# Optimization experiments

Measured on AMD Instinct MI355X. Metric: run time of the kernel, lower is better.

The kernel has to match this reference:

```python
import jax, jax.numpy as jnp
import numpy as np

MIN_VAL = 1e-12  # Ln(min_val=1e-12) in MorphLayer
KSIZE = 3
STRIDE = 1


def _patches(x, k, s):
    # x: (B, C, H, W) -> (B, C*k*k, Ho, Wo), im2col like torch unfold
    return jax.lax.conv_general_dilated_patches(x, (k, k), (s, s), 'VALID')


def _max_plus(p, w):
    # log-domain morphological conv: (B, K, Ho, Wo) + (K, F) -> max over K -> (B, F, Ho, Wo)
    return jnp.max(p[:, :, None, :, :] + w[None, :, :, None, None], axis=1)


def setup_inputs() -> dict:
    key = jax.random.key(0)
    k1, k2, k3 = jax.random.split(key, 3)
    B, C, H, W = 16, 3, 66, 66
    F = 32
    K = C * KSIZE * KSIZE  # 27
    return {
        'x': jax.random.normal(k1, (B, C, H, W), dtype=jnp.float32),
        'kernel_k1': jax.random.normal(k2, (K, F), dtype=jnp.float32) * 0.1,
        'kernel_k2': jax.random.normal(k3, (K, F), dtype=jnp.float32) * 0.1,
        'bias': jnp.zeros((F,), dtype=jnp.float32),
    }


def reference(x, kernel_k1, kernel_k2, bias):
    # Ln: log of positive / negative parts, clamped at MIN_VAL
    x1 = jnp.log(jnp.maximum(x, MIN_VAL))
    x2 = jnp.log(jnp.maximum(-x, MIN_VAL))
    p1 = _patches(x1, KSIZE, STRIDE)  # (B, K, Ho, Wo)
    p2 = _patches(x2, KSIZE, STRIDE)
    y11 = jnp.exp(_max_plus(p1, kernel_k1))
    y12 = jnp.exp(_max_plus(p1, kernel_k2))
    y21 = jnp.exp(_max_plus(p2, kernel_k1))
    y22 = jnp.exp(_max_plus(p2, kernel_k2))
    return y11 - y12 - y21 + y22 + bias[None, :, None, None]
```

## Files before the change

kernel.cpp:

```cpp
#include <hip/hip_runtime.h>
#include <math.h>


#define BB 16
#define CC 3
#define HH 66
#define WW 66
#define HO 64
#define WO 64
#define FF 32
#define KK 27
#define FPB 4
#define FG (FF / FPB)
#define ROWS 4
#define IR (ROWS + 2)
#define LP 68
#define WSTRIDE 56

typedef float f32x2 __attribute__((ext_vector_type(2)));
typedef float f32x4 __attribute__((ext_vector_type(4)));

__global__ __launch_bounds__(256, 8)
void morph_tile(const float* __restrict__ x,
                const float* __restrict__ k1,
                const float* __restrict__ k2,
                const float* __restrict__ bias,
                float* __restrict__ out) {
    __shared__ __align__(16) float xs[CC * IR * LP];
    __shared__ __align__(16) float wl[FPB * WSTRIDE];

    const int tid = threadIdx.x;
    int bid = blockIdx.x;
    const int fg = bid & (FG - 1); bid >>= 3;
    const int rb = bid & 15;       bid >>= 4;
    const int b  = bid;
    const int f0 = fg * FPB;
    const int ho0 = rb * ROWS;

    if (tid < FPB * KK * 2) {
        const int w_  = tid / (KK * 2);
        const int rem = tid - w_ * (KK * 2);
        const int k   = rem >> 1;
        const int h   = rem & 1;
        const float wv = h ? k2[k * FF + f0 + w_] : k1[k * FF + f0 + w_];
        wl[w_ * WSTRIDE + k * 2 + h] = expf(wv);
    }
    const float* xbase = x + (size_t)b * CC * HH * WW;
    for (int i = tid; i < CC * IR * WW; i += 256) {
        const int c   = i / (IR * WW);
        const int rem = i - c * (IR * WW);
        const int row = rem / WW;
        const int col = rem - row * WW;
        xs[(c * IR + row) * LP + col] = xbase[(c * HH + ho0 + row) * WW + col];
    }
    __syncthreads();

    const int w   = tid >> 6;
    const int l   = tid & 63;
    const int rr  = l >> 4;
    const int wo4 = (l & 15) * 4;

    const float* wlw = wl + w * WSTRIDE;
    const int f = f0 + w;

    float m11_0 = 0.f, m11_1 = 0.f, m11_2 = 0.f, m11_3 = 0.f;
    float m12_0 = 0.f, m12_1 = 0.f, m12_2 = 0.f, m12_3 = 0.f;
    float m21_0 = 0.f, m21_1 = 0.f, m21_2 = 0.f, m21_3 = 0.f;
    float m22_0 = 0.f, m22_1 = 0.f, m22_2 = 0.f, m22_3 = 0.f;

#define TAP(k, va, vb, vc, vd) { \
        const f32x2 e = *(const f32x2*)(wlw + (k) * 2);   \
        const f32x2 ab = {va, vb}, cd = {vc, vd}; \
        const f32x2 e1 = {e.x, e.x}, e2 = {e.y, e.y}; \
        const f32x2 p1 = ab * e1, q1 = cd * e1; \
        const f32x2 p2 = ab * e2, q2 = cd * e2; \
        m11_0 = fmaxf(m11_0,  p1.x); m11_1 = fmaxf(m11_1,  p1.y); \
        m11_2 = fmaxf(m11_2,  q1.x); m11_3 = fmaxf(m11_3,  q1.y); \
        m12_0 = fmaxf(m12_0,  p2.x); m12_1 = fmaxf(m12_1,  p2.y); \
        m12_2 = fmaxf(m12_2,  q2.x); m12_3 = fmaxf(m12_3,  q2.y); \
        m21_0 = fmaxf(m21_0, -p1.x); m21_1 = fmaxf(m21_1, -p1.y); \
        m21_2 = fmaxf(m21_2, -q1.x); m21_3 = fmaxf(m21_3, -q1.y); \
        m22_0 = fmaxf(m22_0, -p2.x); m22_1 = fmaxf(m22_1, -p2.y); \
        m22_2 = fmaxf(m22_2, -q2.x); m22_3 = fmaxf(m22_3, -q2.y); \
    }

#define CHUNK(c, di) { \
        const int base_ = ((c * IR + rr + (di)) * LP + wo4); \
        const f32x4 xq = *(const f32x4*)(xs + base_); \
        const f32x2 xr = *(const f32x2*)(xs + base_ + 4); \
        const float s0 = xq.x, s1 = xq.y, s2 = xq.z, s3 = xq.w; \
        const float s4 = xr.x, s5 = xr.y; \
        TAP((c) * 9 + (di) * 3 + 0, s0, s1, s2, s3) \
        TAP((c) * 9 + (di) * 3 + 1, s1, s2, s3, s4) \
        TAP((c) * 9 + (di) * 3 + 2, s2, s3, s4, s5) \
    }

    CHUNK(0, 0) CHUNK(0, 1) CHUNK(0, 2)
    CHUNK(1, 0) CHUNK(1, 1) CHUNK(1, 2)
    CHUNK(2, 0) CHUNK(2, 1) CHUNK(2, 2)
#undef CHUNK
#undef TAP

    const float bs = bias[f];
    f32x4 res;
    res.x = m11_0 - m12_0 - m21_0 + m22_0 + bs;
    res.y = m11_1 - m12_1 - m21_1 + m22_1 + bs;
    res.z = m11_2 - m12_2 - m21_2 + m22_2 + bs;
    res.w = m11_3 - m12_3 - m21_3 + m22_3 + bs;

    *(f32x4*)(out + (((size_t)b * FF + f) * HO + ho0 + rr) * WO + wo4) = res;
}

extern "C" void kernel_launch(void* const* d_in, const int* in_sizes, int n_in,
                              void* d_out, int out_size, void* d_ws, size_t ws_size,
                              hipStream_t stream) {
    const float* x    = (const float*)d_in[0];
    const float* k1   = (const float*)d_in[1];
    const float* k2   = (const float*)d_in[2];
    const float* bias = (const float*)d_in[3];
    float* out = (float*)d_out;

    const int nblocks = BB * (HO / ROWS) * FG;
    morph_tile<<<dim3(nblocks), dim3(256), 0, stream>>>(x, k1, k2, bias, out);
}
```

Before: 14.73 us.

## Compute two output rows per thread with per-channel register window and paired taps

Each thread now computes two output rows instead of one, so a block covers eight rows and half as many blocks are launched. Per channel, the thread loads a 4x8 window from shared memory into registers once and reuses it across both rows and all nine taps. Taps are processed in pairs with nested fmax to shorten dependency chains. This cuts shared-memory loads and per-block staging overhead, but raises register use (launch bounds occupancy hint lowered to 4) and halves grid parallelism.

```diff
diff --git a/kernel.cpp b/kernel.cpp
--- a/kernel.cpp
+++ b/kernel.cpp
@@ -12,15 +12,15 @@
 #define KK 27
 #define FPB 4
 #define FG (FF / FPB)
-#define ROWS 4
-#define IR (ROWS + 2)
+#define OROWS 8
+#define IR (OROWS + 2)
 #define LP 68
 #define WSTRIDE 56
 
 typedef float f32x2 __attribute__((ext_vector_type(2)));
 typedef float f32x4 __attribute__((ext_vector_type(4)));
 
-__global__ __launch_bounds__(256, 8)
+__global__ __launch_bounds__(256, 4)
 void morph_tile(const float* __restrict__ x,
                 const float* __restrict__ k1,
                 const float* __restrict__ k2,
@@ -32,10 +32,10 @@
     const int tid = threadIdx.x;
     int bid = blockIdx.x;
     const int fg = bid & (FG - 1); bid >>= 3;
-    const int rb = bid & 15;       bid >>= 4;
+    const int rb = bid & 7;        bid >>= 3;
     const int b  = bid;
     const int f0 = fg * FPB;
-    const int ho0 = rb * ROWS;
+    const int ho0 = rb * OROWS;
 
     if (tid < FPB * KK * 2) {
         const int w_  = tid / (KK * 2);
@@ -57,58 +57,123 @@
 
     const int w   = tid >> 6;
     const int l   = tid & 63;
-    const int rr  = l >> 4;
+    const int rq  = l >> 4;
     const int wo4 = (l & 15) * 4;
+    const int r0  = rq * 2;
 
     const float* wlw = wl + w * WSTRIDE;
     const int f = f0 + w;
 
-    float m11_0 = 0.f, m11_1 = 0.f, m11_2 = 0.f, m11_3 = 0.f;
-    float m12_0 = 0.f, m12_1 = 0.f, m12_2 = 0.f, m12_3 = 0.f;
-    float m21_0 = 0.f, m21_1 = 0.f, m21_2 = 0.f, m21_3 = 0.f;
-    float m22_0 = 0.f, m22_1 = 0.f, m22_2 = 0.f, m22_3 = 0.f;
+    float m11[2][4], m12[2][4], m21[2][4], m22[2][4];
+    #pragma unroll
+    for (int h = 0; h < 2; ++h)
+        #pragma unroll
+        for (int j = 0; j < 4; ++j) {
+            m11[h][j] = 0.f; m12[h][j] = 0.f; m21[h][j] = 0.f; m22[h][j] = 0.f;
+        }
 
-#define TAP(k, va, vb, vc, vd) { \
-        const f32x2 e = *(const f32x2*)(wlw + (k) * 2);   \
-        const f32x2 ab = {va, vb}, cd = {vc, vd}; \
-        const f32x2 e1 = {e.x, e.x}, e2 = {e.y, e.y}; \
-        const f32x2 p1 = ab * e1, q1 = cd * e1; \
-        const f32x2 p2 = ab * e2, q2 = cd * e2; \
-        m11_0 = fmaxf(m11_0,  p1.x); m11_1 = fmaxf(m11_1,  p1.y); \
-        m11_2 = fmaxf(m11_2,  q1.x); m11_3 = fmaxf(m11_3,  q1.y); \
-        m12_0 = fmaxf(m12_0,  p2.x); m12_1 = fmaxf(m12_1,  p2.y); \
-        m12_2 = fmaxf(m12_2,  q2.x); m12_3 = fmaxf(m12_3,  q2.y); \
-        m21_0 = fmaxf(m21_0, -p1.x); m21_1 = fmaxf(m21_1, -p1.y); \
-        m21_2 = fmaxf(m21_2, -q1.x); m21_3 = fmaxf(m21_3, -q1.y); \
-        m22_0 = fmaxf(m22_0, -p2.x); m22_1 = fmaxf(m22_1, -p2.y); \
-        m22_2 = fmaxf(m22_2, -q2.x); m22_3 = fmaxf(m22_3, -q2.y); \
+    float xw[4][8];
+
+#define LOADCH(c) { \
+        const float* xc_ = xs + ((c) * IR + r0) * LP + wo4; \
+        *(f32x4*)&xw[0][0] = *(const f32x4*)(xc_); \
+        *(f32x4*)&xw[0][4] = *(const f32x4*)(xc_ + 4); \
+        *(f32x4*)&xw[1][0] = *(const f32x4*)(xc_ + LP); \
+        *(f32x4*)&xw[1][4] = *(const f32x4*)(xc_ + LP + 4); \
+        *(f32x4*)&xw[2][0] = *(const f32x4*)(xc_ + 2 * LP); \
+        *(f32x4*)&xw[2][4] = *(const f32x4*)(xc_ + 2 * LP + 4); \
+        *(f32x4*)&xw[3][0] = *(const f32x4*)(xc_ + 3 * LP); \
+        *(f32x4*)&xw[3][4] = *(const f32x4*)(xc_ + 3 * LP + 4); \
     }
 
-#define CHUNK(c, di) { \
-        const int base_ = ((c * IR + rr + (di)) * LP + wo4); \
-        const f32x4 xq = *(const f32x4*)(xs + base_); \
-        const f32x2 xr = *(const f32x2*)(xs + base_ + 4); \
-        const float s0 = xq.x, s1 = xq.y, s2 = xq.z, s3 = xq.w; \
-        const float s4 = xr.x, s5 = xr.y; \
-        TAP((c) * 9 + (di) * 3 + 0, s0, s1, s2, s3) \
-        TAP((c) * 9 + (di) * 3 + 1, s1, s2, s3, s4) \
-        TAP((c) * 9 + (di) * 3 + 2, s2, s3, s4, s5) \
+#define TP_H(h, Ai, Aj, Bi, Bj, e1A, e2A, e1B, e2B) { \
+        const f32x2 pA1 = (f32x2){xw[(Ai)+(h)][(Aj)],   xw[(Ai)+(h)][(Aj)+1]} * e1A; \
+        const f32x2 qA1 = (f32x2){xw[(Ai)+(h)][(Aj)+2], xw[(Ai)+(h)][(Aj)+3]} * e1A; \
+        const f32x2 pA2 = (f32x2){xw[(Ai)+(h)][(Aj)],   xw[(Ai)+(h)][(Aj)+1]} * e2A; \
+        const f32x2 qA2 = (f32x2){xw[(Ai)+(h)][(Aj)+2], xw[(Ai)+(h)][(Aj)+3]} * e2A; \
+        const f32x2 pB1 = (f32x2){xw[(Bi)+(h)][(Bj)],   xw[(Bi)+(h)][(Bj)+1]} * e1B; \
+        const f32x2 qB1 = (f32x2){xw[(Bi)+(h)][(Bj)+2], xw[(Bi)+(h)][(Bj)+3]} * e1B; \
+        const f32x2 pB2 = (f32x2){xw[(Bi)+(h)][(Bj)],   xw[(Bi)+(h)][(Bj)+1]} * e2B; \
+        const f32x2 qB2 = (f32x2){xw[(Bi)+(h)][(Bj)+2], xw[(Bi)+(h)][(Bj)+3]} * e2B; \
+        m11[h][0] = fmaxf(fmaxf(m11[h][0],  pA1.x),  pB1.x); \
+        m11[h][1] = fmaxf(fmaxf(m11[h][1],  pA1.y),  pB1.y); \
+        m11[h][2] = fmaxf(fmaxf(m11[h][2],  qA1.x),  qB1.x); \
+        m11[h][3] = fmaxf(fmaxf(m11[h][3],  qA1.y),  qB1.y); \
+        m12[h][0] = fmaxf(fmaxf(m12[h][0],  pA2.x),  pB2.x); \
+        m12[h][1] = fmaxf(fmaxf(m12[h][1],  pA2.y),  pB2.y); \
+        m12[h][2] = fmaxf(fmaxf(m12[h][2],  qA2.x),  qB2.x); \
+        m12[h][3] = fmaxf(fmaxf(m12[h][3],  qA2.y),  qB2.y); \
+        m21[h][0] = fmaxf(fmaxf(m21[h][0], -pA1.x), -pB1.x); \
+        m21[h][1] = fmaxf(fmaxf(m21[h][1], -pA1.y), -pB1.y); \
+        m21[h][2] = fmaxf(fmaxf(m21[h][2], -qA1.x), -qB1.x); \
+        m21[h][3] = fmaxf(fmaxf(m21[h][3], -qA1.y), -qB1.y); \
+        m22[h][0] = fmaxf(fmaxf(m22[h][0], -pA2.x), -pB2.x); \
+        m22[h][1] = fmaxf(fmaxf(m22[h][1], -pA2.y), -pB2.y); \
+        m22[h][2] = fmaxf(fmaxf(m22[h][2], -qA2.x), -qB2.x); \
+        m22[h][3] = fmaxf(fmaxf(m22[h][3], -qA2.y), -qB2.y); \
     }
 
-    CHUNK(0, 0) CHUNK(0, 1) CHUNK(0, 2)
-    CHUNK(1, 0) CHUNK(1, 1) CHUNK(1, 2)
-    CHUNK(2, 0) CHUNK(2, 1) CHUNK(2, 2)
-#undef CHUNK
-#undef TAP
+#define TAPPAIR(Ai, Aj, Bi, Bj, kA, kB) { \
+        const f32x2 eA_ = *(const f32x2*)(wlw + (kA) * 2); \
+        const f32x2 eB_ = *(const f32x2*)(wlw + (kB) * 2); \
+        const f32x2 e1A = {eA_.x, eA_.x}, e2A = {eA_.y, eA_.y}; \
+        const f32x2 e1B = {eB_.x, eB_.x}, e2B = {eB_.y, eB_.y}; \
+        TP_H(0, Ai, Aj, Bi, Bj, e1A, e2A, e1B, e2B) \
+        TP_H(1, Ai, Aj, Bi, Bj, e1A, e2A, e1B, e2B) \
+    }
+
+#define TS_H(h, Ai, Aj, e1A, e2A) { \
+        const f32x2 p1 = (f32x2){xw[(Ai)+(h)][(Aj)],   xw[(Ai)+(h)][(Aj)+1]} * e1A; \
+        const f32x2 q1 = (f32x2){xw[(Ai)+(h)][(Aj)+2], xw[(Ai)+(h)][(Aj)+3]} * e1A; \
+        const f32x2 p2 = (f32x2){xw[(Ai)+(h)][(Aj)],   xw[(Ai)+(h)][(Aj)+1]} * e2A; \
+        const f32x2 q2 = (f32x2){xw[(Ai)+(h)][(Aj)+2], xw[(Ai)+(h)][(Aj)+3]} * e2A; \
+        m11[h][0] = fmaxf(m11[h][0],  p1.x); m11[h][1] = fmaxf(m11[h][1],  p1.y); \
+        m11[h][2] = fmaxf(m11[h][2],  q1.x); m11[h][3] = fmaxf(m11[h][3],  q1.y); \
+        m12[h][0] = fmaxf(m12[h][0],  p2.x); m12[h][1] = fmaxf(m12[h][1],  p2.y); \
+        m12[h][2] = fmaxf(m12[h][2],  q2.x); m12[h][3] = fmaxf(m12[h][3],  q2.y); \
+        m21[h][0] = fmaxf(m21[h][0], -p1.x); m21[h][1] = fmaxf(m21[h][1], -p1.y); \
+        m21[h][2] = fmaxf(m21[h][2], -q1.x); m21[h][3] = fmaxf(m21[h][3], -q1.y); \
+        m22[h][0] = fmaxf(m22[h][0], -p2.x); m22[h][1] = fmaxf(m22[h][1], -p2.y); \
+        m22[h][2] = fmaxf(m22[h][2], -q2.x); m22[h][3] = fmaxf(m22[h][3], -q2.y); \
+    }
+
+#define TAPSINGLE(Ai, Aj, kA) { \
+        const f32x2 eA_ = *(const f32x2*)(wlw + (kA) * 2); \
+        const f32x2 e1A = {eA_.x, eA_.x}, e2A = {eA_.y, eA_.y}; \
+        TS_H(0, Ai, Aj, e1A, e2A) \
+        TS_H(1, Ai, Aj, e1A, e2A) \
+    }
+
+#define CHANNEL(c) { \
+        LOADCH(c) \
+        TAPPAIR(0, 0, 0, 1, (c)*9 + 0, (c)*9 + 1) \
+        TAPPAIR(0, 2, 1, 0, (c)*9 + 2, (c)*9 + 3) \
+        TAPPAIR(1, 1, 1, 2, (c)*9 + 4, (c)*9 + 5) \
+        TAPPAIR(2, 0, 2, 1, (c)*9 + 6, (c)*9 + 7) \
+        TAPSINGLE(2, 2, (c)*9 + 8) \
+    }
+
+    CHANNEL(0)
+    CHANNEL(1)
+    CHANNEL(2)
+
+#undef CHANNEL
+#undef TAPSINGLE
+#undef TS_H
+#undef TAPPAIR
+#undef TP_H
+#undef LOADCH
 
     const float bs = bias[f];
-    f32x4 res;
-    res.x = m11_0 - m12_0 - m21_0 + m22_0 + bs;
-    res.y = m11_1 - m12_1 - m21_1 + m22_1 + bs;
-    res.z = m11_2 - m12_2 - m21_2 + m22_2 + bs;
-    res.w = m11_3 - m12_3 - m21_3 + m22_3 + bs;
-
-    *(f32x4*)(out + (((size_t)b * FF + f) * HO + ho0 + rr) * WO + wo4) = res;
+    #pragma unroll
+    for (int h = 0; h < 2; ++h) {
+        f32x4 res;
+        res.x = m11[h][0] - m12[h][0] - m21[h][0] + m22[h][0] + bs;
+        res.y = m11[h][1] - m12[h][1] - m21[h][1] + m22[h][1] + bs;
+        res.z = m11[h][2] - m12[h][2] - m21[h][2] + m22[h][2] + bs;
+        res.w = m11[h][3] - m12[h][3] - m21[h][3] + m22[h][3] + bs;
+        *(f32x4*)(out + (((size_t)b * FF + f) * HO + ho0 + r0 + h) * WO + wo4) = res;
+    }
 }
 
 extern "C" void kernel_launch(void* const* d_in, const int* in_sizes, int n_in,
@@ -120,6 +185,6 @@
     const float* bias = (const float*)d_in[3];
     float* out = (float*)d_out;
 
-    const int nblocks = BB * (HO / ROWS) * FG;
+    const int nblocks = BB * (HO / OROWS) * FG;
     morph_tile<<<dim3(nblocks), dim3(256), 0, stream>>>(x, k1, k2, bias, out);
 }
```

Result: no change. 14.48 us (-1.7%).
